# Performance work log

Hardware: AMD Instinct MI355X
Metric: run time of the kernel (lower is better)

## Reference

```python
import jax, jax.numpy as jnp
import numpy as np

B, N1, N2 = 4, 2048, 1024
IN_DIM, OUT_DIM, H = 768, 1024, 16
DH = OUT_DIM // H  # 64
EPS = 1e-5


def _layernorm(x, g, b):
    mu = jnp.mean(x, axis=-1, keepdims=True)
    var = jnp.var(x, axis=-1, keepdims=True)
    return (x - mu) * jax.lax.rsqrt(var + EPS) * g + b


def setup_inputs() -> dict:
    key = jax.random.key(0)
    ks = jax.random.split(key, 16)
    s_in = 1.0 / np.sqrt(IN_DIM)
    s_out = 1.0 / np.sqrt(OUT_DIM)
    return {
        "input": jax.random.normal(ks[0], (B, N1, IN_DIM), jnp.float32),
        "output": jax.random.normal(ks[1], (B, N2, OUT_DIM), jnp.float32),
        "q_w": jax.random.uniform(ks[2], (OUT_DIM, OUT_DIM), jnp.float32, -s_out, s_out),
        "q_b": jax.random.uniform(ks[3], (OUT_DIM,), jnp.float32, -s_out, s_out),
        "k_w": jax.random.uniform(ks[4], (OUT_DIM, IN_DIM), jnp.float32, -s_in, s_in),
        "k_b": jax.random.uniform(ks[5], (OUT_DIM,), jnp.float32, -s_in, s_in),
        "v_w": jax.random.uniform(ks[6], (OUT_DIM, IN_DIM), jnp.float32, -s_in, s_in),
        "v_b": jax.random.uniform(ks[7], (OUT_DIM,), jnp.float32, -s_in, s_in),
        "proj_w": jax.random.uniform(ks[8], (OUT_DIM, OUT_DIM), jnp.float32, -s_out, s_out),
        "proj_b": jax.random.uniform(ks[9], (OUT_DIM,), jnp.float32, -s_out, s_out),
        "ln_in_g": jnp.ones((IN_DIM,), jnp.float32),
        "ln_in_b": jnp.zeros((IN_DIM,), jnp.float32),
        "ln_out_g": jnp.ones((OUT_DIM,), jnp.float32),
        "ln_out_b": jnp.zeros((OUT_DIM,), jnp.float32),
    }


def reference(input, output, q_w, q_b, k_w, k_b, v_w, v_b, proj_w, proj_b,
              ln_in_g, ln_in_b, ln_out_g, ln_out_b):
    i = _layernorm(input, ln_in_g, ln_in_b)            # [B,N1,IN]
    o = _layernorm(output, ln_out_g, ln_out_b)         # [B,N2,OUT]
    q = (o @ q_w.T + q_b).reshape(B, N2, H, DH)        # [B,N2,H,DH]
    k = (i @ k_w.T + k_b).reshape(B, N1, H, DH)
    v = (i @ v_w.T + v_b).reshape(B, N1, H, DH)
    scores = jnp.einsum("bqhd,bkhd->bhqk", q, k) / np.sqrt(DH).astype(np.float32)
    att_probs = jax.nn.softmax(scores, axis=-1)        # [B,H,N2,N1]
    ctrl = jnp.einsum("bhqk,bkhd->bqhd", att_probs, v).reshape(B, N2, OUT_DIM)
    out = output + (ctrl @ proj_w.T + proj_b)          # residual (DropPath p=0 is identity)
    return (att_probs, out)
```

## Files before the change

### kernel.cpp

```cpp
#include <hip/hip_runtime.h>
#include <hip/hip_bf16.h>
#include <math.h>


typedef __attribute__((ext_vector_type(8))) short short8;
typedef __attribute__((ext_vector_type(4))) float f32x4;

__device__ __forceinline__ ushort f2b(float f) {
  __hip_bfloat16 h = __float2bfloat16(f);
  return *reinterpret_cast<ushort*>(&h);
}

__device__ __forceinline__ void gload16(const ushort* g, ushort* lds) {
  __builtin_amdgcn_global_load_lds(
      (const __attribute__((address_space(1))) unsigned int*)g,
      (__attribute__((address_space(3))) unsigned int*)lds, 16, 0, 0);
}

__global__ __launch_bounds__(256) void cvt_kernel(const float* __restrict__ src,
                                                  ushort* __restrict__ dst,
                                                  int n4) {
  int i = blockIdx.x * 256 + threadIdx.x;
  if (i >= n4) return;
  float4 v = ((const float4*)src)[i];
  ushort4 o;
  o.x = f2b(v.x); o.y = f2b(v.y); o.z = f2b(v.z); o.w = f2b(v.w);
  ((ushort4*)dst)[i] = o;
}

__device__ __forceinline__ float wave_red_sum(float v) {
#pragma unroll
  for (int o = 32; o; o >>= 1) v += __shfl_down(v, o);
  return v;
}

__global__ __launch_bounds__(256) void ln_kernel(
    const float* __restrict__ src, const float* __restrict__ g,
    const float* __restrict__ bta, ushort* __restrict__ dst, int D) {
  size_t row = blockIdx.x;
  const float* x = src + row * (size_t)D;
  ushort* y = dst + row * (size_t)D;
  int nv = D >> 2;
  float s = 0.f, s2 = 0.f;
  for (int i = threadIdx.x; i < nv; i += 256) {
    float4 v = ((const float4*)x)[i];
    s += v.x + v.y + v.z + v.w;
    s2 += v.x * v.x + v.y * v.y + v.z * v.z + v.w * v.w;
  }
  s = wave_red_sum(s);
  s2 = wave_red_sum(s2);
  __shared__ float red[8];
  int wid = threadIdx.x >> 6, lane = threadIdx.x & 63;
  if (lane == 0) { red[wid] = s; red[4 + wid] = s2; }
  __syncthreads();
  float ts = red[0] + red[1] + red[2] + red[3];
  float t2 = red[4] + red[5] + red[6] + red[7];
  float mu = ts / (float)D;
  float rstd = rsqrtf(t2 / (float)D - mu * mu + 1e-5f);
  for (int i = threadIdx.x; i < nv; i += 256) {
    float4 v = ((const float4*)x)[i];
    float4 gg = ((const float4*)g)[i];
    float4 bb = ((const float4*)bta)[i];
    ushort4 o;
    o.x = f2b((v.x - mu) * rstd * gg.x + bb.x);
    o.y = f2b((v.y - mu) * rstd * gg.y + bb.y);
    o.z = f2b((v.z - mu) * rstd * gg.z + bb.z);
    o.w = f2b((v.w - mu) * rstd * gg.w + bb.w);
    ((ushort4*)y)[i] = o;
  }
}

template <bool CBF, int BIASMODE, bool RES>
__global__ __launch_bounds__(256) void gemm_bf16(
    const ushort* __restrict__ A, const ushort* __restrict__ W,
    const float* __restrict__ bias, const float* __restrict__ resid, void* Cv,
    int K, int lda, int ldw, int ldc, long long sA1, long long sA2,
    long long sW1, long long sW2, long long sC1, long long sC2, int zdiv,
    float alpha) {
  __shared__ __align__(16) ushort As[2][128 * 32];
  __shared__ __align__(16) ushort Ws[2][64 * 32];
  int z = blockIdx.z;
  int zb = z / zdiv, zh = z % zdiv;
  const ushort* Ab = A + (size_t)zb * sA1 + (size_t)zh * sA2 +
                     (size_t)blockIdx.x * 128 * lda;
  const ushort* Wb = W + (size_t)zb * sW1 + (size_t)zh * sW2 +
                     (size_t)blockIdx.y * 64 * ldw;
  int tid = threadIdx.x, l = tid & 63, w = tid >> 6;
  int wr = w >> 1, wc = w & 1;
  f32x4 acc[4][2];
#pragma unroll
  for (int i = 0; i < 4; ++i)
#pragma unroll
    for (int j = 0; j < 2; ++j) acc[i][j] = (f32x4){0.f, 0.f, 0.f, 0.f};

  int srow = l >> 2, scol = (l & 3) * 8;
  int lr = l & 15, lk = (l >> 4) * 8;

#define STAGE(bb, k0)                                                       \
  do {                                                                      \
    const ushort* ga = Ab + (size_t)(w * 32 + srow) * lda + (k0) + scol;    \
    gload16(ga, &As[bb][(w * 32) * 32]);                                    \
    gload16(ga + (size_t)16 * lda, &As[bb][(w * 32 + 16) * 32]);            \
    gload16(Wb + (size_t)(w * 16 + srow) * ldw + (k0) + scol,               \
            &Ws[bb][(w * 16) * 32]);                                        \
  } while (0)

  int nk = K >> 5;
  STAGE(0, 0);
  for (int t = 0; t < nk; ++t) {
    int cur = t & 1;
    if (t + 1 < nk) {
      STAGE(cur ^ 1, (t + 1) * 32);
      asm volatile("s_waitcnt vmcnt(3)" ::: "memory");
    } else {
      asm volatile("s_waitcnt vmcnt(0)" ::: "memory");
    }
    __builtin_amdgcn_s_barrier();
    __builtin_amdgcn_sched_barrier(0);
    short8 af[4], bf[2];
#pragma unroll
    for (int fi = 0; fi < 4; ++fi)
      af[fi] = *(const short8*)&As[cur][(wr * 64 + fi * 16 + lr) * 32 + lk];
#pragma unroll
    for (int fj = 0; fj < 2; ++fj)
      bf[fj] = *(const short8*)&Ws[cur][(wc * 32 + fj * 16 + lr) * 32 + lk];
    __builtin_amdgcn_s_setprio(1);
#pragma unroll
    for (int fi = 0; fi < 4; ++fi)
#pragma unroll
      for (int fj = 0; fj < 2; ++fj)
        acc[fi][fj] = __builtin_amdgcn_mfma_f32_16x16x32_bf16(
            af[fi], bf[fj], acc[fi][fj], 0, 0, 0);
    __builtin_amdgcn_s_setprio(0);
    __builtin_amdgcn_s_barrier();
  }
#undef STAGE

  int m0 = blockIdx.x * 128, n0 = blockIdx.y * 64;
  size_t cb = (size_t)zb * sC1 + (size_t)zh * sC2;
#pragma unroll
  for (int fi = 0; fi < 4; ++fi)
#pragma unroll
    for (int fj = 0; fj < 2; ++fj) {
      int col = n0 + wc * 32 + fj * 16 + lr;
      float bv = 0.f;
      if (BIASMODE == 1) bv = bias[col];
#pragma unroll
      for (int r4 = 0; r4 < 4; ++r4) {
        int row = m0 + wr * 64 + fi * 16 + (l >> 4) * 4 + r4;
        float val = acc[fi][fj][r4] * alpha + bv;
        if (BIASMODE == 2) val += bias[row];
        if (RES) val += resid[(size_t)row * ldc + col];
        if (CBF)
          ((ushort*)Cv)[cb + (size_t)row * ldc + col] = f2b(val);
        else
          ((float*)Cv)[cb + (size_t)row * ldc + col] = val;
      }
    }
}

__global__ __launch_bounds__(256, 3) void attn_kernel(
    const ushort* __restrict__ qb, const ushort* __restrict__ kb,
    const ushort* __restrict__ vt, float* __restrict__ att,
    ushort* __restrict__ ctrl) {
  __shared__ ushort QP_lds[64 * 72];
  __shared__ ushort K_lds[2][64 * 72];
  __shared__ ushort V_lds[2][64 * 72];

  int bid = blockIdx.x;
  int vv = ((bid & 7) << 7) + (bid >> 3);
  int bh = vv >> 4, mt = vv & 15;
  int b = bh >> 4, h = bh & 15;
  int m0 = mt * 64;
  int tid = threadIdx.x, l = tid & 63, w = tid >> 6;
  int lr = l & 15, lk = (l >> 4) * 8;
  int klo = (l >> 4) * 4;

  const float SC = 0.125f * 1.44269504088896f;

#pragma unroll
  for (int it = 0; it < 2; ++it) {
    int idx = tid + it * 256;
    int row = idx >> 3, c8 = (idx & 7) * 8;
    *(uint4*)&QP_lds[row * 72 + c8] = *(const uint4*)(
        qb + (size_t)(b * 1024 + m0 + row) * 1024 + h * 64 + c8);
  }
  __syncthreads();
  short8 aq0 = *(const short8*)&QP_lds[(w * 16 + lr) * 72 + lk];
  short8 aq1 = *(const short8*)&QP_lds[(w * 16 + lr) * 72 + 32 + lk];
  __syncthreads();

  const size_t kbase = (size_t)b * 2048 * 1024 + h * 64;
  const ushort* Kb = kb + kbase;
  int srow = tid >> 3, sc8 = (tid & 7) * 8;

  float mrow = -1e30f, lsum = 0.f;

  uint4 kr0 = *(const uint4*)(Kb + (size_t)srow * 1024 + sc8);
  uint4 kr1 = *(const uint4*)(Kb + (size_t)(srow + 32) * 1024 + sc8);
  for (int t = 0; t < 32; ++t) {
    int cur = t & 1;
    *(uint4*)&K_lds[cur][srow * 72 + sc8] = kr0;
    *(uint4*)&K_lds[cur][(srow + 32) * 72 + sc8] = kr1;
    asm volatile("s_waitcnt lgkmcnt(0)" ::: "memory");
    __builtin_amdgcn_s_barrier();
    __builtin_amdgcn_sched_barrier(0);
    if (t < 31) {
      kr0 = *(const uint4*)(Kb + (size_t)(t * 64 + 64 + srow) * 1024 + sc8);
      kr1 = *(const uint4*)(Kb + (size_t)(t * 64 + 96 + srow) * 1024 + sc8);
    }
    f32x4 acc[4];
    __builtin_amdgcn_s_setprio(1);
#pragma unroll
    for (int fj = 0; fj < 4; ++fj) {
      short8 kf0 = *(const short8*)&K_lds[cur][(fj * 16 + lr) * 72 + lk];
      short8 kf1 = *(const short8*)&K_lds[cur][(fj * 16 + lr) * 72 + 32 + lk];
      f32x4 a = (f32x4){0.f, 0.f, 0.f, 0.f};
      a = __builtin_amdgcn_mfma_f32_16x16x32_bf16(kf0, aq0, a, 0, 0, 0);
      a = __builtin_amdgcn_mfma_f32_16x16x32_bf16(kf1, aq1, a, 0, 0, 0);
      acc[fj] = a;
    }
    __builtin_amdgcn_s_setprio(0);
    float cm = mrow;
#pragma unroll
    for (int fj = 0; fj < 4; ++fj) {
      float a01 = fmaxf(acc[fj][0], acc[fj][1]);
      float a23 = fmaxf(acc[fj][2], acc[fj][3]);
      cm = fmaxf(cm, fmaxf(a01, a23) * SC);
    }
    cm = fmaxf(cm, __shfl_xor(cm, 16));
    cm = fmaxf(cm, __shfl_xor(cm, 32));
    float cs = 0.f;
#pragma unroll
    for (int fj = 0; fj < 4; ++fj)
#pragma unroll
      for (int r = 0; r < 4; ++r) cs += exp2f(fmaf(acc[fj][r], SC, -cm));
    cs += __shfl_xor(cs, 16);
    cs += __shfl_xor(cs, 32);
    lsum = lsum * exp2f(mrow - cm) + cs;
    mrow = cm;
  }
  float mb = mrow + __log2f(lsum);

  float* attp = att + (size_t)bh * 2048 * 1024 + (size_t)m0 * 2048;
  const ushort* Vb = vt + (size_t)bh * 64 * 2048;
  int qrow = w * 16 + lr;
  f32x4 acco[4];
#pragma unroll
  for (int fd = 0; fd < 4; ++fd) acco[fd] = (f32x4){0.f, 0.f, 0.f, 0.f};

  kr0 = *(const uint4*)(Kb + (size_t)srow * 1024 + sc8);
  kr1 = *(const uint4*)(Kb + (size_t)(srow + 32) * 1024 + sc8);
  uint4 vr0 = *(const uint4*)(Vb + (size_t)srow * 2048 + sc8);
  uint4 vr1 = *(const uint4*)(Vb + (size_t)(srow + 32) * 2048 + sc8);
  for (int t = 0; t < 32; ++t) {
    int cur = t & 1;
    int k0 = t * 64;
    *(uint4*)&K_lds[cur][srow * 72 + sc8] = kr0;
    *(uint4*)&K_lds[cur][(srow + 32) * 72 + sc8] = kr1;
    *(uint4*)&V_lds[cur][srow * 72 + sc8] = vr0;
    *(uint4*)&V_lds[cur][(srow + 32) * 72 + sc8] = vr1;
    asm volatile("s_waitcnt lgkmcnt(0)" ::: "memory");
    __builtin_amdgcn_s_barrier();
    __builtin_amdgcn_sched_barrier(0);
    if (t < 31) {
      kr0 = *(const uint4*)(Kb + (size_t)(k0 + 64 + srow) * 1024 + sc8);
      kr1 = *(const uint4*)(Kb + (size_t)(k0 + 96 + srow) * 1024 + sc8);
      vr0 = *(const uint4*)(Vb + (size_t)srow * 2048 + k0 + 64 + sc8);
      vr1 = *(const uint4*)(Vb + (size_t)(srow + 32) * 2048 + k0 + 64 + sc8);
    }
    f32x4 acc[4];
    __builtin_amdgcn_s_setprio(1);
#pragma unroll
    for (int fj = 0; fj < 4; ++fj) {
      short8 kf0 = *(const short8*)&K_lds[cur][(fj * 16 + lr) * 72 + lk];
      short8 kf1 = *(const short8*)&K_lds[cur][(fj * 16 + lr) * 72 + 32 + lk];
      f32x4 a = (f32x4){0.f, 0.f, 0.f, 0.f};
      a = __builtin_amdgcn_mfma_f32_16x16x32_bf16(kf0, aq0, a, 0, 0, 0);
      a = __builtin_amdgcn_mfma_f32_16x16x32_bf16(kf1, aq1, a, 0, 0, 0);
      acc[fj] = a;
    }
    __builtin_amdgcn_s_setprio(0);
#pragma unroll
    for (int fj = 0; fj < 4; ++fj) {
      float4 p;
      p.x = exp2f(fmaf(acc[fj][0], SC, -mb));
      p.y = exp2f(fmaf(acc[fj][1], SC, -mb));
      p.z = exp2f(fmaf(acc[fj][2], SC, -mb));
      p.w = exp2f(fmaf(acc[fj][3], SC, -mb));
      *(float4*)(attp + (size_t)qrow * 2048 + k0 + fj * 16 + klo) = p;
      union { uint2 u; ushort s[4]; } pk;
      pk.s[0] = f2b(p.x);
      pk.s[1] = f2b(p.y);
      pk.s[2] = f2b(p.z);
      pk.s[3] = f2b(p.w);
      *(uint2*)&QP_lds[qrow * 72 + fj * 16 + klo] = pk.u;
    }
    short8 ap0 = *(const short8*)&QP_lds[(w * 16 + lr) * 72 + lk];
    short8 ap1 = *(const short8*)&QP_lds[(w * 16 + lr) * 72 + 32 + lk];
    __builtin_amdgcn_s_setprio(1);
#pragma unroll
    for (int fd = 0; fd < 4; ++fd) {
      short8 bv0 = *(const short8*)&V_lds[cur][(fd * 16 + lr) * 72 + lk];
      short8 bv1 = *(const short8*)&V_lds[cur][(fd * 16 + lr) * 72 + 32 + lk];
      acco[fd] =
          __builtin_amdgcn_mfma_f32_16x16x32_bf16(ap0, bv0, acco[fd], 0, 0, 0);
      acco[fd] =
          __builtin_amdgcn_mfma_f32_16x16x32_bf16(ap1, bv1, acco[fd], 0, 0, 0);
    }
    __builtin_amdgcn_s_setprio(0);
  }

#pragma unroll
  for (int fd = 0; fd < 4; ++fd)
#pragma unroll
    for (int r = 0; r < 4; ++r) {
      int wrow = w * 16 + (l >> 4) * 4 + r;
      ctrl[(size_t)(b * 1024 + m0 + wrow) * 1024 + h * 64 + fd * 16 + lr] =
          f2b(acco[fd][r]);
    }
}

extern "C" void kernel_launch(void* const* d_in, const int* in_sizes, int n_in,
                              void* d_out, int out_size, void* d_ws,
                              size_t ws_size, hipStream_t stream) {
  const float* input = (const float*)d_in[0];
  const float* output = (const float*)d_in[1];
  const float* q_w = (const float*)d_in[2];
  const float* q_b = (const float*)d_in[3];
  const float* k_w = (const float*)d_in[4];
  const float* k_b = (const float*)d_in[5];
  const float* v_w = (const float*)d_in[6];
  const float* v_b = (const float*)d_in[7];
  const float* p_w = (const float*)d_in[8];
  const float* p_b = (const float*)d_in[9];
  const float* ln_in_g = (const float*)d_in[10];
  const float* ln_in_b = (const float*)d_in[11];
  const float* ln_out_g = (const float*)d_in[12];
  const float* ln_out_b = (const float*)d_in[13];

  ushort* ws = (ushort*)d_ws;
  ushort* i_ln = ws;
  ushort* o_ln = i_ln + 6291456;
  ushort* qb = o_ln + 4194304;
  ushort* kb = qb + 4194304;
  ushort* vt = kb + 8388608;
  ushort* ctrl = vt + 8388608;
  ushort* qwb = ctrl + 4194304;
  ushort* kwb = qwb + 1048576;
  ushort* vwb = kwb + 786432;
  ushort* pwb = vwb + 786432;

  float* att = (float*)d_out;
  float* out2 = att + 134217728LL;

  cvt_kernel<<<1024, 256, 0, stream>>>(q_w, qwb, 262144);
  cvt_kernel<<<768, 256, 0, stream>>>(k_w, kwb, 196608);
  cvt_kernel<<<768, 256, 0, stream>>>(v_w, vwb, 196608);
  cvt_kernel<<<1024, 256, 0, stream>>>(p_w, pwb, 262144);

  ln_kernel<<<8192, 256, 0, stream>>>(input, ln_in_g, ln_in_b, i_ln, 768);
  ln_kernel<<<4096, 256, 0, stream>>>(output, ln_out_g, ln_out_b, o_ln, 1024);

  gemm_bf16<true, 1, false><<<dim3(32, 16, 1), 256, 0, stream>>>(
      o_ln, qwb, q_b, nullptr, qb, 1024, 1024, 1024, 1024, 0, 0, 0, 0, 0, 0,
      1, 1.0f);
  gemm_bf16<true, 1, false><<<dim3(64, 16, 1), 256, 0, stream>>>(
      i_ln, kwb, k_b, nullptr, kb, 768, 768, 768, 1024, 0, 0, 0, 0, 0, 0, 1,
      1.0f);
  gemm_bf16<true, 2, false><<<dim3(8, 32, 4), 256, 0, stream>>>(
      vwb, i_ln, v_b, nullptr, vt, 768, 768, 768, 2048, 0, 0,
      (long long)2048 * 768, 0, (long long)1024 * 2048, 0, 1, 1.0f);

  attn_kernel<<<dim3(1024), 256, 0, stream>>>(qb, kb, vt, att, ctrl);

  gemm_bf16<false, 1, true><<<dim3(32, 16, 1), 256, 0, stream>>>(
      ctrl, pwb, p_b, output, out2, 1024, 1024, 1024, 1024, 0, 0, 0, 0, 0, 0,
      1, 1.0f);
}
```

Before: 336.1 us.

## Split attention into stats and emit kernels, drop LDS staging, merge small launches

Splits the two-pass attention kernel into a stats kernel that computes the per-row log-sum-exp into a workspace buffer and an emit kernel that writes the probabilities and accumulates P·V. Both kernels now read K and V fragments straight from global memory rather than staging them through double-buffered LDS with barriers, and they use a higher occupancy target. The probability output is written with nontemporal stores, and the four weight conversions and two layernorms are each merged into a single launch. The aim is to cut barrier and launch overhead and keep the large probability write out of the caches, at the cost of uncoalesced, repeated global loads of K and V.

Result: slower. 467.3 us (+39.0%).

```diff
diff --git a/kernel.cpp b/kernel.cpp
--- a/kernel.cpp
+++ b/kernel.cpp
@@ -17,15 +17,23 @@
       (__attribute__((address_space(3))) unsigned int*)lds, 16, 0, 0);
 }
 
-__global__ __launch_bounds__(256) void cvt_kernel(const float* __restrict__ src,
-                                                  ushort* __restrict__ dst,
-                                                  int n4) {
+__global__ __launch_bounds__(256) void cvt4_kernel(
+    const float* __restrict__ s0, ushort* __restrict__ d0,
+    const float* __restrict__ s1, ushort* __restrict__ d1,
+    const float* __restrict__ s2, ushort* __restrict__ d2,
+    const float* __restrict__ s3, ushort* __restrict__ d3) {
   int i = blockIdx.x * 256 + threadIdx.x;
-  if (i >= n4) return;
-  float4 v = ((const float4*)src)[i];
+  const float* s;
+  ushort* d;
+  int j = i;
+  if (i < 262144) { s = s0; d = d0; }
+  else if (i < 458752) { s = s1; d = d1; j = i - 262144; }
+  else if (i < 655360) { s = s2; d = d2; j = i - 458752; }
+  else { s = s3; d = d3; j = i - 655360; }
+  float4 v = ((const float4*)s)[j];
   ushort4 o;
   o.x = f2b(v.x); o.y = f2b(v.y); o.z = f2b(v.z); o.w = f2b(v.w);
-  ((ushort4*)dst)[i] = o;
+  ((ushort4*)d)[j] = o;
 }
 
 __device__ __forceinline__ float wave_red_sum(float v) {
@@ -34,12 +42,10 @@
   return v;
 }
 
-__global__ __launch_bounds__(256) void ln_kernel(
-    const float* __restrict__ src, const float* __restrict__ g,
-    const float* __restrict__ bta, ushort* __restrict__ dst, int D) {
-  size_t row = blockIdx.x;
-  const float* x = src + row * (size_t)D;
-  ushort* y = dst + row * (size_t)D;
+__device__ __forceinline__ void ln_row(const float* __restrict__ x,
+                                       const float* __restrict__ g,
+                                       const float* __restrict__ bta,
+                                       ushort* __restrict__ y, int D) {
   int nv = D >> 2;
   float s = 0.f, s2 = 0.f;
   for (int i = threadIdx.x; i < nv; i += 256) {
@@ -70,6 +76,20 @@
   }
 }
 
+__global__ __launch_bounds__(256) void ln2_kernel(
+    const float* __restrict__ inA, const float* __restrict__ gA,
+    const float* __restrict__ bA, ushort* __restrict__ yA,
+    const float* __restrict__ inB, const float* __restrict__ gB,
+    const float* __restrict__ bB, ushort* __restrict__ yB) {
+  size_t r = blockIdx.x;
+  if (r < 8192)
+    ln_row(inA + r * 768, gA, bA, yA + r * 768, 768);
+  else {
+    size_t rr = r - 8192;
+    ln_row(inB + rr * 1024, gB, bB, yB + rr * 1024, 1024);
+  }
+}
+
 template <bool CBF, int BIASMODE, bool RES>
 __global__ __launch_bounds__(256) void gemm_bf16(
     const ushort* __restrict__ A, const ushort* __restrict__ W,
@@ -159,13 +179,66 @@
     }
 }
 
-__global__ __launch_bounds__(256, 3) void attn_kernel(
+__global__ __launch_bounds__(256, 4) void stats_kernel(
     const ushort* __restrict__ qb, const ushort* __restrict__ kb,
-    const ushort* __restrict__ vt, float* __restrict__ att,
-    ushort* __restrict__ ctrl) {
-  __shared__ ushort QP_lds[64 * 72];
-  __shared__ ushort K_lds[2][64 * 72];
-  __shared__ ushort V_lds[2][64 * 72];
+    float* __restrict__ mbuf) {
+  int bid = blockIdx.x;
+  int vv = ((bid & 7) << 7) + (bid >> 3);
+  int bh = vv >> 4, mt = vv & 15;
+  int b = bh >> 4, h = bh & 15;
+  int m0 = mt * 64;
+  int tid = threadIdx.x, l = tid & 63, w = tid >> 6;
+  int lr = l & 15, lk = (l >> 4) * 8;
+  const float SC = 0.125f * 1.44269504088896f;
+
+  int qrow = w * 16 + lr;
+  const ushort* Qp = qb + (size_t)(b * 1024 + m0 + qrow) * 1024 + h * 64;
+  short8 aq0 = *(const short8*)(Qp + lk);
+  short8 aq1 = *(const short8*)(Qp + 32 + lk);
+
+  const ushort* Kb = kb + (size_t)b * 2048 * 1024 + h * 64;
+  float mrow = -1e30f, lsum = 0.f;
+  for (int t = 0; t < 32; ++t) {
+    int k0 = t * 64;
+    f32x4 acc[4];
+#pragma unroll
+    for (int fj = 0; fj < 4; ++fj) {
+      const ushort* kp = Kb + (size_t)(k0 + fj * 16 + lr) * 1024;
+      short8 kf0 = *(const short8*)(kp + lk);
+      short8 kf1 = *(const short8*)(kp + 32 + lk);
+      f32x4 a = (f32x4){0.f, 0.f, 0.f, 0.f};
+      a = __builtin_amdgcn_mfma_f32_16x16x32_bf16(kf0, aq0, a, 0, 0, 0);
+      a = __builtin_amdgcn_mfma_f32_16x16x32_bf16(kf1, aq1, a, 0, 0, 0);
+      acc[fj] = a;
+    }
+    float cm = mrow;
+#pragma unroll
+    for (int fj = 0; fj < 4; ++fj) {
+      float a01 = fmaxf(acc[fj][0], acc[fj][1]);
+      float a23 = fmaxf(acc[fj][2], acc[fj][3]);
+      cm = fmaxf(cm, fmaxf(a01, a23) * SC);
+    }
+    cm = fmaxf(cm, __shfl_xor(cm, 16));
+    cm = fmaxf(cm, __shfl_xor(cm, 32));
+    float cs = 0.f;
+#pragma unroll
+    for (int fj = 0; fj < 4; ++fj)
+#pragma unroll
+      for (int r = 0; r < 4; ++r) cs += exp2f(fmaf(acc[fj][r], SC, -cm));
+    cs += __shfl_xor(cs, 16);
+    cs += __shfl_xor(cs, 32);
+    lsum = lsum * exp2f(mrow - cm) + cs;
+    mrow = cm;
+  }
+  float mb = mrow + __log2f(lsum);
+  if (l < 16) mbuf[(size_t)bh * 1024 + m0 + w * 16 + l] = mb;
+}
+
+__global__ __launch_bounds__(256, 4) void emit_kernel(
+    const ushort* __restrict__ qb, const ushort* __restrict__ kb,
+    const ushort* __restrict__ vt, const float* __restrict__ mbuf,
+    float* __restrict__ att, ushort* __restrict__ ctrl) {
+  __shared__ ushort P_lds[64 * 72];
 
   int bid = blockIdx.x;
   int vv = ((bid & 7) << 7) + (bid >> 3);
@@ -175,140 +248,63 @@
   int tid = threadIdx.x, l = tid & 63, w = tid >> 6;
   int lr = l & 15, lk = (l >> 4) * 8;
   int klo = (l >> 4) * 4;
-
   const float SC = 0.125f * 1.44269504088896f;
 
-#pragma unroll
-  for (int it = 0; it < 2; ++it) {
-    int idx = tid + it * 256;
-    int row = idx >> 3, c8 = (idx & 7) * 8;
-    *(uint4*)&QP_lds[row * 72 + c8] = *(const uint4*)(
-        qb + (size_t)(b * 1024 + m0 + row) * 1024 + h * 64 + c8);
-  }
-  __syncthreads();
-  short8 aq0 = *(const short8*)&QP_lds[(w * 16 + lr) * 72 + lk];
-  short8 aq1 = *(const short8*)&QP_lds[(w * 16 + lr) * 72 + 32 + lk];
-  __syncthreads();
-
-  const size_t kbase = (size_t)b * 2048 * 1024 + h * 64;
-  const ushort* Kb = kb + kbase;
-  int srow = tid >> 3, sc8 = (tid & 7) * 8;
-
-  float mrow = -1e30f, lsum = 0.f;
-
-  uint4 kr0 = *(const uint4*)(Kb + (size_t)srow * 1024 + sc8);
-  uint4 kr1 = *(const uint4*)(Kb + (size_t)(srow + 32) * 1024 + sc8);
+  int qrow = w * 16 + lr;
+  const ushort* Qp = qb + (size_t)(b * 1024 + m0 + qrow) * 1024 + h * 64;
+  short8 aq0 = *(const short8*)(Qp + lk);
+  short8 aq1 = *(const short8*)(Qp + 32 + lk);
+  float mb = mbuf[(size_t)bh * 1024 + m0 + qrow];
+
+  const ushort* Kb = kb + (size_t)b * 2048 * 1024 + h * 64;
+  const ushort* Vb = vt + (size_t)bh * 64 * 2048;
+  float* attp = att + (size_t)bh * 2048 * 1024 + (size_t)m0 * 2048;
+
+  f32x4 acco[4];
+#pragma unroll
+  for (int fd = 0; fd < 4; ++fd) acco[fd] = (f32x4){0.f, 0.f, 0.f, 0.f};
+
   for (int t = 0; t < 32; ++t) {
-    int cur = t & 1;
-    *(uint4*)&K_lds[cur][srow * 72 + sc8] = kr0;
-    *(uint4*)&K_lds[cur][(srow + 32) * 72 + sc8] = kr1;
-    asm volatile("s_waitcnt lgkmcnt(0)" ::: "memory");
-    __builtin_amdgcn_s_barrier();
-    __builtin_amdgcn_sched_barrier(0);
-    if (t < 31) {
-      kr0 = *(const uint4*)(Kb + (size_t)(t * 64 + 64 + srow) * 1024 + sc8);
-      kr1 = *(const uint4*)(Kb + (size_t)(t * 64 + 96 + srow) * 1024 + sc8);
-    }
+    int k0 = t * 64;
     f32x4 acc[4];
-    __builtin_amdgcn_s_setprio(1);
 #pragma unroll
     for (int fj = 0; fj < 4; ++fj) {
-      short8 kf0 = *(const short8*)&K_lds[cur][(fj * 16 + lr) * 72 + lk];
-      short8 kf1 = *(const short8*)&K_lds[cur][(fj * 16 + lr) * 72 + 32 + lk];
+      const ushort* kp = Kb + (size_t)(k0 + fj * 16 + lr) * 1024;
+      short8 kf0 = *(const short8*)(kp + lk);
+      short8 kf1 = *(const short8*)(kp + 32 + lk);
       f32x4 a = (f32x4){0.f, 0.f, 0.f, 0.f};
       a = __builtin_amdgcn_mfma_f32_16x16x32_bf16(kf0, aq0, a, 0, 0, 0);
       a = __builtin_amdgcn_mfma_f32_16x16x32_bf16(kf1, aq1, a, 0, 0, 0);
       acc[fj] = a;
     }
-    __builtin_amdgcn_s_setprio(0);
-    float cm = mrow;
 #pragma unroll
     for (int fj = 0; fj < 4; ++fj) {
-      float a01 = fmaxf(acc[fj][0], acc[fj][1]);
-      float a23 = fmaxf(acc[fj][2], acc[fj][3]);
-      cm = fmaxf(cm, fmaxf(a01, a23) * SC);
-    }
-    cm = fmaxf(cm, __shfl_xor(cm, 16));
-    cm = fmaxf(cm, __shfl_xor(cm, 32));
-    float cs = 0.f;
-#pragma unroll
-    for (int fj = 0; fj < 4; ++fj)
-#pragma unroll
-      for (int r = 0; r < 4; ++r) cs += exp2f(fmaf(acc[fj][r], SC, -cm));
-    cs += __shfl_xor(cs, 16);
-    cs += __shfl_xor(cs, 32);
-    lsum = lsum * exp2f(mrow - cm) + cs;
-    mrow = cm;
-  }
-  float mb = mrow + __log2f(lsum);
-
-  float* attp = att + (size_t)bh * 2048 * 1024 + (size_t)m0 * 2048;
-  const ushort* Vb = vt + (size_t)bh * 64 * 2048;
-  int qrow = w * 16 + lr;
-  f32x4 acco[4];
-#pragma unroll
-  for (int fd = 0; fd < 4; ++fd) acco[fd] = (f32x4){0.f, 0.f, 0.f, 0.f};
-
-  kr0 = *(const uint4*)(Kb + (size_t)srow * 1024 + sc8);
-  kr1 = *(const uint4*)(Kb + (size_t)(srow + 32) * 1024 + sc8);
-  uint4 vr0 = *(const uint4*)(Vb + (size_t)srow * 2048 + sc8);
-  uint4 vr1 = *(const uint4*)(Vb + (size_t)(srow + 32) * 2048 + sc8);
-  for (int t = 0; t < 32; ++t) {
-    int cur = t & 1;
-    int k0 = t * 64;
-    *(uint4*)&K_lds[cur][srow * 72 + sc8] = kr0;
-    *(uint4*)&K_lds[cur][(srow + 32) * 72 + sc8] = kr1;
-    *(uint4*)&V_lds[cur][srow * 72 + sc8] = vr0;
-    *(uint4*)&V_lds[cur][(srow + 32) * 72 + sc8] = vr1;
-    asm volatile("s_waitcnt lgkmcnt(0)" ::: "memory");
-    __builtin_amdgcn_s_barrier();
-    __builtin_amdgcn_sched_barrier(0);
-    if (t < 31) {
-      kr0 = *(const uint4*)(Kb + (size_t)(k0 + 64 + srow) * 1024 + sc8);
-      kr1 = *(const uint4*)(Kb + (size_t)(k0 + 96 + srow) * 1024 + sc8);
-      vr0 = *(const uint4*)(Vb + (size_t)srow * 2048 + k0 + 64 + sc8);
-      vr1 = *(const uint4*)(Vb + (size_t)(srow + 32) * 2048 + k0 + 64 + sc8);
-    }
-    f32x4 acc[4];
-    __builtin_amdgcn_s_setprio(1);
-#pragma unroll
-    for (int fj = 0; fj < 4; ++fj) {
-      short8 kf0 = *(const short8*)&K_lds[cur][(fj * 16 + lr) * 72 + lk];
-      short8 kf1 = *(const short8*)&K_lds[cur][(fj * 16 + lr) * 72 + 32 + lk];
-      f32x4 a = (f32x4){0.f, 0.f, 0.f, 0.f};
-      a = __builtin_amdgcn_mfma_f32_16x16x32_bf16(kf0, aq0, a, 0, 0, 0);
-      a = __builtin_amdgcn_mfma_f32_16x16x32_bf16(kf1, aq1, a, 0, 0, 0);
-      acc[fj] = a;
-    }
-    __builtin_amdgcn_s_setprio(0);
-#pragma unroll
-    for (int fj = 0; fj < 4; ++fj) {
-      float4 p;
-      p.x = exp2f(fmaf(acc[fj][0], SC, -mb));
-      p.y = exp2f(fmaf(acc[fj][1], SC, -mb));
-      p.z = exp2f(fmaf(acc[fj][2], SC, -mb));
-      p.w = exp2f(fmaf(acc[fj][3], SC, -mb));
-      *(float4*)(attp + (size_t)qrow * 2048 + k0 + fj * 16 + klo) = p;
+      f32x4 p;
+      p[0] = exp2f(fmaf(acc[fj][0], SC, -mb));
+      p[1] = exp2f(fmaf(acc[fj][1], SC, -mb));
+      p[2] = exp2f(fmaf(acc[fj][2], SC, -mb));
+      p[3] = exp2f(fmaf(acc[fj][3], SC, -mb));
+      __builtin_nontemporal_store(
+          p, (f32x4*)(attp + (size_t)qrow * 2048 + k0 + fj * 16 + klo));
       union { uint2 u; ushort s[4]; } pk;
-      pk.s[0] = f2b(p.x);
-      pk.s[1] = f2b(p.y);
-      pk.s[2] = f2b(p.z);
-      pk.s[3] = f2b(p.w);
-      *(uint2*)&QP_lds[qrow * 72 + fj * 16 + klo] = pk.u;
-    }
-    short8 ap0 = *(const short8*)&QP_lds[(w * 16 + lr) * 72 + lk];
-    short8 ap1 = *(const short8*)&QP_lds[(w * 16 + lr) * 72 + 32 + lk];
-    __builtin_amdgcn_s_setprio(1);
+      pk.s[0] = f2b(p[0]);
+      pk.s[1] = f2b(p[1]);
+      pk.s[2] = f2b(p[2]);
+      pk.s[3] = f2b(p[3]);
+      *(uint2*)&P_lds[qrow * 72 + fj * 16 + klo] = pk.u;
+    }
+    short8 ap0 = *(const short8*)&P_lds[qrow * 72 + lk];
+    short8 ap1 = *(const short8*)&P_lds[qrow * 72 + 32 + lk];
 #pragma unroll
     for (int fd = 0; fd < 4; ++fd) {
-      short8 bv0 = *(const short8*)&V_lds[cur][(fd * 16 + lr) * 72 + lk];
-      short8 bv1 = *(const short8*)&V_lds[cur][(fd * 16 + lr) * 72 + 32 + lk];
+      const ushort* vp = Vb + (size_t)(fd * 16 + lr) * 2048 + k0;
+      short8 bv0 = *(const short8*)(vp + lk);
+      short8 bv1 = *(const short8*)(vp + 32 + lk);
       acco[fd] =
           __builtin_amdgcn_mfma_f32_16x16x32_bf16(ap0, bv0, acco[fd], 0, 0, 0);
       acco[fd] =
           __builtin_amdgcn_mfma_f32_16x16x32_bf16(ap1, bv1, acco[fd], 0, 0, 0);
     }
-    __builtin_amdgcn_s_setprio(0);
   }
 
 #pragma unroll
@@ -350,17 +346,15 @@
   ushort* kwb = qwb + 1048576;
   ushort* vwb = kwb + 786432;
   ushort* pwb = vwb + 786432;
+  float* mbuf = (float*)(pwb + 1048576);
 
   float* att = (float*)d_out;
   float* out2 = att + 134217728LL;
 
-  cvt_kernel<<<1024, 256, 0, stream>>>(q_w, qwb, 262144);
-  cvt_kernel<<<768, 256, 0, stream>>>(k_w, kwb, 196608);
-  cvt_kernel<<<768, 256, 0, stream>>>(v_w, vwb, 196608);
-  cvt_kernel<<<1024, 256, 0, stream>>>(p_w, pwb, 262144);
-
-  ln_kernel<<<8192, 256, 0, stream>>>(input, ln_in_g, ln_in_b, i_ln, 768);
-  ln_kernel<<<4096, 256, 0, stream>>>(output, ln_out_g, ln_out_b, o_ln, 1024);
+  cvt4_kernel<<<3584, 256, 0, stream>>>(q_w, qwb, k_w, kwb, v_w, vwb, p_w,
+                                        pwb);
+  ln2_kernel<<<12288, 256, 0, stream>>>(input, ln_in_g, ln_in_b, i_ln, output,
+                                        ln_out_g, ln_out_b, o_ln);
 
   gemm_bf16<true, 1, false><<<dim3(32, 16, 1), 256, 0, stream>>>(
       o_ln, qwb, q_b, nullptr, qb, 1024, 1024, 1024, 1024, 0, 0, 0, 0, 0, 0,
@@ -372,7 +366,8 @@
       vwb, i_ln, v_b, nullptr, vt, 768, 768, 768, 2048, 0, 0,
       (long long)2048 * 768, 0, (long long)1024 * 2048, 0, 1, 1.0f);
 
-  attn_kernel<<<dim3(1024), 256, 0, stream>>>(qb, kb, vt, att, ctrl);
+  stats_kernel<<<dim3(1024), 256, 0, stream>>>(qb, kb, mbuf);
+  emit_kernel<<<dim3(1024), 256, 0, stream>>>(qb, kb, vt, mbuf, att, ctrl);
 
   gemm_bf16<false, 1, true><<<dim3(32, 16, 1), 256, 0, stream>>>(
       ctrl, pwb, p_b, output, out2, 1024, 1024, 1024, 1024, 0, 0, 0, 0, 0, 0,
```
